# Kernel optimization log

Hardware: AMD Instinct MI355X
Metric: run time of the kernel (lower is better)

The kernel has to match this reference:

```python
import jax, jax.numpy as jnp
import numpy as np

N_NODES = 50000
N_EDGES = 800000
IN_FT = 256
OUT_FT = 128


def setup_inputs() -> dict:
    key = jax.random.key(0)
    k_seq, k_src, k_dst, k_val, k_w = jax.random.split(key, 5)
    seq = jax.random.normal(k_seq, (N_NODES, IN_FT), dtype=jnp.float32)
    edge_src = jax.random.randint(k_src, (N_EDGES,), 0, N_NODES, dtype=jnp.int64)
    edge_dst = jax.random.randint(k_dst, (N_EDGES,), 0, N_NODES, dtype=jnp.int64)
    edge_val = jax.random.uniform(k_val, (N_EDGES,), dtype=jnp.float32)
    # xavier_uniform for Linear(in_ft, out_ft): limit = sqrt(6/(in+out))
    limit = float(np.sqrt(6.0 / (IN_FT + OUT_FT)))
    W = jax.random.uniform(k_w, (OUT_FT, IN_FT), minval=-limit, maxval=limit, dtype=jnp.float32)
    bias = jnp.zeros((OUT_FT,), dtype=jnp.float32)
    prelu_a = jnp.full((1,), 0.25, dtype=jnp.float32)  # nn.PReLU default slope
    return {"seq": seq, "edge_src": edge_src, "edge_dst": edge_dst,
            "edge_val": edge_val, "W": W, "bias": bias, "prelu_a": prelu_a}


def reference(seq, edge_src, edge_dst, edge_val, W, bias, prelu_a):
    # seq_fts = fc(seq): [N, out_ft]
    seq_fts = jnp.einsum('ni,oi->no', seq, W)
    # sparse spmm: out[dst] += val * seq_fts[src]
    msgs = seq_fts[edge_src] * edge_val[:, None]          # [E, out_ft]
    out = jax.ops.segment_sum(msgs, edge_dst, num_segments=seq.shape[0])
    out = out + bias                                       # bias add
    # PReLU with learnable slope a
    return jnp.where(out >= 0, out, prelu_a * out)
```

## Files before the change

### kernel.cpp

```cpp
#include <hip/hip_runtime.h>
#include <hip/hip_bf16.h>

#define N_NODES 50000
#define N_EDGES 800000
#define IN_FT 256
#define OUT_FT 128

typedef __bf16 bf16;
typedef __attribute__((ext_vector_type(8))) __bf16 bf16x8;
typedef __attribute__((ext_vector_type(4))) float floatx4;

static __device__ inline unsigned short f2bf_bits(float f) {
    unsigned u = __float_as_uint(f);
    return (unsigned short)((u + 0x7FFFu + ((u >> 16) & 1u)) >> 16);
}

#define SLOT_LG 6
#define SLOTS (1 << SLOT_LG)
#define BKN 128
#define NBUCK 392
#define NPAD (NBUCK * BKN)
#define EPB 2048
#define NBLK_A ((N_EDGES + EPB - 1) / EPB)
#define CELL 32
#define SXCAP 2560
#define GM 128
#define GEMM_BLKS ((N_NODES + GM - 1) / GM)
#define WP 264
#define SMEM_BYTES (128 * WP * 2)

__global__ __launch_bounds__(512) void k_ga(const float* __restrict__ seq,
                                            const float* __restrict__ W,
                                            unsigned short* __restrict__ seq_fts,
                                            const int* __restrict__ src,
                                            const int* __restrict__ dst,
                                            const float* __restrict__ val,
                                            int* __restrict__ cnt,
                                            uint2* __restrict__ part) {
    const int t = threadIdx.x;
    __shared__ __align__(16) char smem[SMEM_BYTES];
    if (blockIdx.x < GEMM_BLKS) {
        bf16* Wlds = (bf16*)smem;
        {
            const int row = t >> 2, c0 = (t & 3) * 64;
            const float* wsrc = W + row * IN_FT + c0;
            unsigned short* dstp = (unsigned short*)(Wlds + row * WP + c0);
#pragma unroll
            for (int c = 0; c < 16; ++c) {
                float4 v = *(const float4*)(wsrc + c * 4);
                ushort4 o;
                o.x = f2bf_bits(v.x); o.y = f2bf_bits(v.y);
                o.z = f2bf_bits(v.z); o.w = f2bf_bits(v.w);
                *(ushort4*)(dstp + c * 4) = o;
            }
        }
        const int lane = t & 63;
        const int wave = t >> 6;
        const int quad = lane >> 4;
        const int l16  = lane & 15;

        int arow = blockIdx.x * GM + wave * 16 + l16;
        if (arow >= N_NODES) arow = 0;
        const float* ap = seq + (size_t)arow * IN_FT + quad * 8;
        bf16x8 afr[8];
#pragma unroll
        for (int s = 0; s < 8; ++s) {
            float4 v0 = *(const float4*)(ap + s * 32);
            float4 v1 = *(const float4*)(ap + s * 32 + 4);
            bf16x8 a;
            a[0] = (bf16)v0.x; a[1] = (bf16)v0.y; a[2] = (bf16)v0.z; a[3] = (bf16)v0.w;
            a[4] = (bf16)v1.x; a[5] = (bf16)v1.y; a[6] = (bf16)v1.z; a[7] = (bf16)v1.w;
            afr[s] = a;
        }
        __syncthreads();

        const int mbase = blockIdx.x * GM + wave * 16;
#pragma unroll
        for (int tt = 0; tt < 8; ++tt) {
            floatx4 acc = {0.f, 0.f, 0.f, 0.f};
            const bf16* bp = Wlds + (tt * 16 + l16) * WP + quad * 8;
#pragma unroll
            for (int s = 0; s < 8; ++s) {
                bf16x8 bfr = *(const bf16x8*)(bp + s * 32);
                acc = __builtin_amdgcn_mfma_f32_16x16x32_bf16(afr[s], bfr, acc, 0, 0, 0);
            }
#pragma unroll
            for (int r = 0; r < 4; ++r) {
                int m = mbase + quad * 4 + r;
                if (m < N_NODES)
                    seq_fts[(size_t)m * OUT_FT + tt * 16 + l16] = f2bf_bits(acc[r]);
            }
        }
    } else {
        int*   h     = (int*)smem;
        int*   lbase = h + NBUCK;
        int*   sc    = lbase + NBUCK;
        uint2* srt   = (uint2*)(sc + 512);

        const int B2 = blockIdx.x - GEMM_BLKS;
        const int e0 = B2 * EPB;
        if (t < NBUCK) h[t] = 0;
        __syncthreads();

        int      myd[4];
        int      myofs[4];
        unsigned myx[4];
#pragma unroll
        for (int k = 0; k < 4; ++k) {
            int e = e0 + k * 512 + t;
            int d = (e < N_EDGES) ? dst[e] : -1;
            myd[k] = d;
            if (d >= 0) {
                myx[k] = (unsigned)(unsigned short)src[e]
                       | ((unsigned)f2bf_bits(val[e]) << 16);
                myofs[k] = atomicAdd(&h[d >> 7], 1);
            }
        }
        __syncthreads();
        int v = (t < NBUCK) ? min(h[t], CELL) : 0;
        sc[t] = v;
        __syncthreads();
        for (int s = 1; s < 512; s <<= 1) {
            int a = (t >= s) ? sc[t - s] : 0;
            __syncthreads();
            sc[t] += a;
            __syncthreads();
        }
        if (t < NBUCK) { lbase[t] = sc[t] - v; cnt[t * NBLK_A + B2] = v; }
        __syncthreads();
        const int total = sc[NBUCK - 1];
#pragma unroll
        for (int k = 0; k < 4; ++k) {
            int d = myd[k];
            if (d >= 0 && myofs[k] < CELL)
                srt[lbase[d >> 7] + myofs[k]] = make_uint2(myx[k], (unsigned)d);
        }
        __syncthreads();
        for (int i = t; i < total; i += 512) {
            uint2 r = srt[i];
            int bb = (int)(r.y >> 7);
            part[(size_t)(bb * NBLK_A + B2) * CELL + (unsigned)(i - lbase[bb])] = r;
        }
    }
}

__global__ __launch_bounds__(512) void k_B(const int* __restrict__ cnt,
                                           const uint2* __restrict__ part,
                                           unsigned* __restrict__ csr_ev,
                                           int* __restrict__ deg) {
    const int b = blockIdx.x, t = threadIdx.x;
    __shared__ int sc[512];
    __shared__ int ncnt[BKN], nbase[BKN], ncur[BKN];
    __shared__ int tot_sh;
    __shared__ unsigned fx[SXCAP];
    __shared__ unsigned char fdn[SXCAP];
    __shared__ unsigned sx[SXCAP];
    __shared__ unsigned char sdn[SXCAP];

    if (t < BKN) ncnt[t] = 0;
    const int len = (t < NBLK_A) ? cnt[b * NBLK_A + t] : 0;
    sc[t] = len;
    __syncthreads();
    for (int s = 1; s < 512; s <<= 1) {
        int a = (t >= s) ? sc[t - s] : 0;
        __syncthreads();
        sc[t] += a;
        __syncthreads();
    }
    const int cellbase = sc[t] - len;
    if (t == NBLK_A - 1) tot_sh = sc[NBLK_A - 1];
    __syncthreads();
    const int totc = (tot_sh < SXCAP) ? tot_sh : SXCAP;

    if (t < NBLK_A) {
        const uint2* cp = part + (size_t)(b * NBLK_A + t) * CELL;
        for (int k = 0; k < len; ++k) {
            int idx = cellbase + k;
            if (idx < SXCAP) {
                uint2 r = cp[k];
                int dn = (int)(r.y & (BKN - 1));
                fx[idx] = r.x;
                fdn[idx] = (unsigned char)dn;
                atomicAdd(&ncnt[dn], 1);
            }
        }
    }
    __syncthreads();
    int v2 = (t < BKN) ? ncnt[t] : 0;
    if (t < BKN) sc[t] = v2;
    __syncthreads();
    for (int s = 1; s < BKN; s <<= 1) {
        int a = (t < BKN && t >= s) ? sc[t - s] : 0;
        __syncthreads();
        if (t < BKN) sc[t] += a;
        __syncthreads();
    }
    if (t < BKN) {
        nbase[t] = sc[t] - v2;
        ncur[t]  = sc[t] - v2;
        deg[b * BKN + t] = (v2 < SLOTS) ? v2 : SLOTS;
    }
    __syncthreads();
    for (int i = t; i < totc; i += 512) {
        unsigned x = fx[i];
        int dn = fdn[i];
        int j = atomicAdd(&ncur[dn], 1);
        sx[j] = x; sdn[j] = (unsigned char)dn;
    }
    __syncthreads();
    for (int j = t; j < totc; j += 512) {
        int dn = sdn[j];
        int lpos = j - nbase[dn];
        if (lpos < SLOTS)
            csr_ev[((unsigned)(b * BKN + dn) << SLOT_LG) + (unsigned)lpos] = sx[j];
    }
}

#define GW 4
__global__ __launch_bounds__(64 * GW) void k_gather(const unsigned* __restrict__ fts,
                                                    const int* __restrict__ deg,
                                                    const unsigned* __restrict__ csr_ev,
                                                    const float* __restrict__ bias,
                                                    const float* __restrict__ prelu_a,
                                                    float* __restrict__ out) {
    const int wave = threadIdx.x >> 6;
    const int lane = threadIdx.x & 63;
    const int n = blockIdx.x * GW + wave;
    if (n >= N_NODES) return;
    const int d = deg[n];
    const int s0 = n << SLOT_LG;
    const int s1 = s0 + d;
    float acc0 = 0.f, acc1 = 0.f;
    int j = s0;
    for (; j + 7 < s1; j += 8) {
        uint4 ca = *(const uint4*)&csr_ev[j];
        uint4 cb = *(const uint4*)&csr_ev[j + 4];
        unsigned q0 = fts[(ca.x & 0xFFFFu) * 64u + lane];
        unsigned q1 = fts[(ca.y & 0xFFFFu) * 64u + lane];
        unsigned q2 = fts[(ca.z & 0xFFFFu) * 64u + lane];
        unsigned q3 = fts[(ca.w & 0xFFFFu) * 64u + lane];
        unsigned q4 = fts[(cb.x & 0xFFFFu) * 64u + lane];
        unsigned q5 = fts[(cb.y & 0xFFFFu) * 64u + lane];
        unsigned q6 = fts[(cb.z & 0xFFFFu) * 64u + lane];
        unsigned q7 = fts[(cb.w & 0xFFFFu) * 64u + lane];
        acc0 += __uint_as_float(ca.x & 0xFFFF0000u) * __uint_as_float(q0 << 16);
        acc1 += __uint_as_float(ca.x & 0xFFFF0000u) * __uint_as_float(q0 & 0xFFFF0000u);
        acc0 += __uint_as_float(ca.y & 0xFFFF0000u) * __uint_as_float(q1 << 16);
        acc1 += __uint_as_float(ca.y & 0xFFFF0000u) * __uint_as_float(q1 & 0xFFFF0000u);
        acc0 += __uint_as_float(ca.z & 0xFFFF0000u) * __uint_as_float(q2 << 16);
        acc1 += __uint_as_float(ca.z & 0xFFFF0000u) * __uint_as_float(q2 & 0xFFFF0000u);
        acc0 += __uint_as_float(ca.w & 0xFFFF0000u) * __uint_as_float(q3 << 16);
        acc1 += __uint_as_float(ca.w & 0xFFFF0000u) * __uint_as_float(q3 & 0xFFFF0000u);
        acc0 += __uint_as_float(cb.x & 0xFFFF0000u) * __uint_as_float(q4 << 16);
        acc1 += __uint_as_float(cb.x & 0xFFFF0000u) * __uint_as_float(q4 & 0xFFFF0000u);
        acc0 += __uint_as_float(cb.y & 0xFFFF0000u) * __uint_as_float(q5 << 16);
        acc1 += __uint_as_float(cb.y & 0xFFFF0000u) * __uint_as_float(q5 & 0xFFFF0000u);
        acc0 += __uint_as_float(cb.z & 0xFFFF0000u) * __uint_as_float(q6 << 16);
        acc1 += __uint_as_float(cb.z & 0xFFFF0000u) * __uint_as_float(q6 & 0xFFFF0000u);
        acc0 += __uint_as_float(cb.w & 0xFFFF0000u) * __uint_as_float(q7 << 16);
        acc1 += __uint_as_float(cb.w & 0xFFFF0000u) * __uint_as_float(q7 & 0xFFFF0000u);
    }
    for (; j + 3 < s1; j += 4) {
        uint4 ca = *(const uint4*)&csr_ev[j];
        unsigned q0 = fts[(ca.x & 0xFFFFu) * 64u + lane];
        unsigned q1 = fts[(ca.y & 0xFFFFu) * 64u + lane];
        unsigned q2 = fts[(ca.z & 0xFFFFu) * 64u + lane];
        unsigned q3 = fts[(ca.w & 0xFFFFu) * 64u + lane];
        acc0 += __uint_as_float(ca.x & 0xFFFF0000u) * __uint_as_float(q0 << 16);
        acc1 += __uint_as_float(ca.x & 0xFFFF0000u) * __uint_as_float(q0 & 0xFFFF0000u);
        acc0 += __uint_as_float(ca.y & 0xFFFF0000u) * __uint_as_float(q1 << 16);
        acc1 += __uint_as_float(ca.y & 0xFFFF0000u) * __uint_as_float(q1 & 0xFFFF0000u);
        acc0 += __uint_as_float(ca.z & 0xFFFF0000u) * __uint_as_float(q2 << 16);
        acc1 += __uint_as_float(ca.z & 0xFFFF0000u) * __uint_as_float(q2 & 0xFFFF0000u);
        acc0 += __uint_as_float(ca.w & 0xFFFF0000u) * __uint_as_float(q3 << 16);
        acc1 += __uint_as_float(ca.w & 0xFFFF0000u) * __uint_as_float(q3 & 0xFFFF0000u);
    }
    for (; j < s1; ++j) {
        unsigned w0 = csr_ev[j];
        unsigned p0 = fts[(w0 & 0xFFFFu) * 64u + lane];
        float v0 = __uint_as_float(w0 & 0xFFFF0000u);
        acc0 += v0 * __uint_as_float(p0 << 16);
        acc1 += v0 * __uint_as_float(p0 & 0xFFFF0000u);
    }
    float2 bb = *(const float2*)&bias[lane * 2];
    float a = prelu_a[0];
    float x0 = acc0 + bb.x;
    float x1 = acc1 + bb.y;
    x0 = (x0 >= 0.f) ? x0 : a * x0;
    x1 = (x1 >= 0.f) ? x1 : a * x1;
    *(float2*)&out[(size_t)n * OUT_FT + lane * 2] = make_float2(x0, x1);
}

extern "C" void kernel_launch(void* const* d_in, const int* in_sizes, int n_in,
                              void* d_out, int out_size, void* d_ws, size_t ws_size,
                              hipStream_t stream) {
    const float* seq      = (const float*)d_in[0];
    const int*   edge_src = (const int*)d_in[1];
    const int*   edge_dst = (const int*)d_in[2];
    const float* edge_val = (const float*)d_in[3];
    const float* W        = (const float*)d_in[4];
    const float* bias     = (const float*)d_in[5];
    const float* prelu_a  = (const float*)d_in[6];
    float* out = (float*)d_out;

    char* ws = (char*)d_ws;
    size_t off = 0;
    auto alloc = [&](size_t bytes) {
        void* p = ws + off;
        off = (off + bytes + 255) & ~(size_t)255;
        return p;
    };
    unsigned short* seq_fts = (unsigned short*)alloc((size_t)N_NODES * OUT_FT * sizeof(unsigned short));
    int*      cnt    = (int*)alloc((size_t)NBUCK * NBLK_A * sizeof(int));
    uint2*    part   = (uint2*)alloc((size_t)NBUCK * NBLK_A * CELL * sizeof(uint2));
    unsigned* csr_ev = (unsigned*)alloc((size_t)NPAD * SLOTS * sizeof(unsigned));
    int*      deg    = (int*)alloc((size_t)NPAD * sizeof(int));
    (void)ws_size; (void)in_sizes; (void)n_in; (void)out_size;

    k_ga<<<GEMM_BLKS + NBLK_A, 512, 0, stream>>>(seq, W, seq_fts,
                                                 edge_src, edge_dst, edge_val,
                                                 cnt, part);
    k_B<<<NBUCK, 512, 0, stream>>>(cnt, part, csr_ev, deg);
    k_gather<<<(N_NODES + GW - 1) / GW, 64 * GW, 0, stream>>>((const unsigned*)seq_fts,
                                                              deg, csr_ev,
                                                              bias, prelu_a, out);
}
```

Before: 169.5 us.

## Fuse bucket sort and gather into one kernel reading edges from LDS

Merges the per-bucket local sort kernel and the per-node gather kernel into one 1024-thread kernel. After the sort, 16 waves per block walk the 128 nodes of the bucket, reading edge records straight from shared memory. This drops the padded global CSR buffer, the degree array, their global write and read round trip, and one kernel launch. It also removes the 64-edge per-node cap. In exchange the gather runs with only 392 large blocks instead of many small ones, which lowers parallelism and load balancing for a latency-bound random gather.

```diff
diff --git a/kernel.cpp b/kernel.cpp
--- a/kernel.cpp
+++ b/kernel.cpp
@@ -15,8 +15,6 @@
     return (unsigned short)((u + 0x7FFFu + ((u >> 16) & 1u)) >> 16);
 }
 
-#define SLOT_LG 6
-#define SLOTS (1 << SLOT_LG)
 #define BKN 128
 #define NBUCK 392
 #define NPAD (NBUCK * BKN)
@@ -144,12 +142,15 @@
     }
 }
 
-__global__ __launch_bounds__(512) void k_B(const int* __restrict__ cnt,
-                                           const uint2* __restrict__ part,
-                                           unsigned* __restrict__ csr_ev,
-                                           int* __restrict__ deg) {
+#define NW 16
+__global__ __launch_bounds__(1024) void k_BG(const int* __restrict__ cnt,
+                                             const uint2* __restrict__ part,
+                                             const unsigned* __restrict__ fts,
+                                             const float* __restrict__ bias,
+                                             const float* __restrict__ prelu_a,
+                                             float* __restrict__ out) {
     const int b = blockIdx.x, t = threadIdx.x;
-    __shared__ int sc[512];
+    __shared__ int sc[1024];
     __shared__ int ncnt[BKN], nbase[BKN], ncur[BKN];
     __shared__ int tot_sh;
     __shared__ unsigned fx[SXCAP];
@@ -198,97 +199,86 @@
     if (t < BKN) {
         nbase[t] = sc[t] - v2;
         ncur[t]  = sc[t] - v2;
-        deg[b * BKN + t] = (v2 < SLOTS) ? v2 : SLOTS;
-    }
-    __syncthreads();
-    for (int i = t; i < totc; i += 512) {
+    }
+    __syncthreads();
+    for (int i = t; i < totc; i += 1024) {
         unsigned x = fx[i];
         int dn = fdn[i];
         int j = atomicAdd(&ncur[dn], 1);
         sx[j] = x; sdn[j] = (unsigned char)dn;
     }
     __syncthreads();
-    for (int j = t; j < totc; j += 512) {
-        int dn = sdn[j];
-        int lpos = j - nbase[dn];
-        if (lpos < SLOTS)
-            csr_ev[((unsigned)(b * BKN + dn) << SLOT_LG) + (unsigned)lpos] = sx[j];
-    }
-}
-
-#define GW 4
-__global__ __launch_bounds__(64 * GW) void k_gather(const unsigned* __restrict__ fts,
-                                                    const int* __restrict__ deg,
-                                                    const unsigned* __restrict__ csr_ev,
-                                                    const float* __restrict__ bias,
-                                                    const float* __restrict__ prelu_a,
-                                                    float* __restrict__ out) {
-    const int wave = threadIdx.x >> 6;
-    const int lane = threadIdx.x & 63;
-    const int n = blockIdx.x * GW + wave;
-    if (n >= N_NODES) return;
-    const int d = deg[n];
-    const int s0 = n << SLOT_LG;
-    const int s1 = s0 + d;
-    float acc0 = 0.f, acc1 = 0.f;
-    int j = s0;
-    for (; j + 7 < s1; j += 8) {
-        uint4 ca = *(const uint4*)&csr_ev[j];
-        uint4 cb = *(const uint4*)&csr_ev[j + 4];
-        unsigned q0 = fts[(ca.x & 0xFFFFu) * 64u + lane];
-        unsigned q1 = fts[(ca.y & 0xFFFFu) * 64u + lane];
-        unsigned q2 = fts[(ca.z & 0xFFFFu) * 64u + lane];
-        unsigned q3 = fts[(ca.w & 0xFFFFu) * 64u + lane];
-        unsigned q4 = fts[(cb.x & 0xFFFFu) * 64u + lane];
-        unsigned q5 = fts[(cb.y & 0xFFFFu) * 64u + lane];
-        unsigned q6 = fts[(cb.z & 0xFFFFu) * 64u + lane];
-        unsigned q7 = fts[(cb.w & 0xFFFFu) * 64u + lane];
-        acc0 += __uint_as_float(ca.x & 0xFFFF0000u) * __uint_as_float(q0 << 16);
-        acc1 += __uint_as_float(ca.x & 0xFFFF0000u) * __uint_as_float(q0 & 0xFFFF0000u);
-        acc0 += __uint_as_float(ca.y & 0xFFFF0000u) * __uint_as_float(q1 << 16);
-        acc1 += __uint_as_float(ca.y & 0xFFFF0000u) * __uint_as_float(q1 & 0xFFFF0000u);
-        acc0 += __uint_as_float(ca.z & 0xFFFF0000u) * __uint_as_float(q2 << 16);
-        acc1 += __uint_as_float(ca.z & 0xFFFF0000u) * __uint_as_float(q2 & 0xFFFF0000u);
-        acc0 += __uint_as_float(ca.w & 0xFFFF0000u) * __uint_as_float(q3 << 16);
-        acc1 += __uint_as_float(ca.w & 0xFFFF0000u) * __uint_as_float(q3 & 0xFFFF0000u);
-        acc0 += __uint_as_float(cb.x & 0xFFFF0000u) * __uint_as_float(q4 << 16);
-        acc1 += __uint_as_float(cb.x & 0xFFFF0000u) * __uint_as_float(q4 & 0xFFFF0000u);
-        acc0 += __uint_as_float(cb.y & 0xFFFF0000u) * __uint_as_float(q5 << 16);
-        acc1 += __uint_as_float(cb.y & 0xFFFF0000u) * __uint_as_float(q5 & 0xFFFF0000u);
-        acc0 += __uint_as_float(cb.z & 0xFFFF0000u) * __uint_as_float(q6 << 16);
-        acc1 += __uint_as_float(cb.z & 0xFFFF0000u) * __uint_as_float(q6 & 0xFFFF0000u);
-        acc0 += __uint_as_float(cb.w & 0xFFFF0000u) * __uint_as_float(q7 << 16);
-        acc1 += __uint_as_float(cb.w & 0xFFFF0000u) * __uint_as_float(q7 & 0xFFFF0000u);
-    }
-    for (; j + 3 < s1; j += 4) {
-        uint4 ca = *(const uint4*)&csr_ev[j];
-        unsigned q0 = fts[(ca.x & 0xFFFFu) * 64u + lane];
-        unsigned q1 = fts[(ca.y & 0xFFFFu) * 64u + lane];
-        unsigned q2 = fts[(ca.z & 0xFFFFu) * 64u + lane];
-        unsigned q3 = fts[(ca.w & 0xFFFFu) * 64u + lane];
-        acc0 += __uint_as_float(ca.x & 0xFFFF0000u) * __uint_as_float(q0 << 16);
-        acc1 += __uint_as_float(ca.x & 0xFFFF0000u) * __uint_as_float(q0 & 0xFFFF0000u);
-        acc0 += __uint_as_float(ca.y & 0xFFFF0000u) * __uint_as_float(q1 << 16);
-        acc1 += __uint_as_float(ca.y & 0xFFFF0000u) * __uint_as_float(q1 & 0xFFFF0000u);
-        acc0 += __uint_as_float(ca.z & 0xFFFF0000u) * __uint_as_float(q2 << 16);
-        acc1 += __uint_as_float(ca.z & 0xFFFF0000u) * __uint_as_float(q2 & 0xFFFF0000u);
-        acc0 += __uint_as_float(ca.w & 0xFFFF0000u) * __uint_as_float(q3 << 16);
-        acc1 += __uint_as_float(ca.w & 0xFFFF0000u) * __uint_as_float(q3 & 0xFFFF0000u);
-    }
-    for (; j < s1; ++j) {
-        unsigned w0 = csr_ev[j];
-        unsigned p0 = fts[(w0 & 0xFFFFu) * 64u + lane];
-        float v0 = __uint_as_float(w0 & 0xFFFF0000u);
-        acc0 += v0 * __uint_as_float(p0 << 16);
-        acc1 += v0 * __uint_as_float(p0 & 0xFFFF0000u);
-    }
-    float2 bb = *(const float2*)&bias[lane * 2];
-    float a = prelu_a[0];
-    float x0 = acc0 + bb.x;
-    float x1 = acc1 + bb.y;
-    x0 = (x0 >= 0.f) ? x0 : a * x0;
-    x1 = (x1 >= 0.f) ? x1 : a * x1;
-    *(float2*)&out[(size_t)n * OUT_FT + lane * 2] = make_float2(x0, x1);
+
+    const int wave = t >> 6;
+    const int lane = t & 63;
+    const float2 bb2 = *(const float2*)&bias[lane * 2];
+    const float a = prelu_a[0];
+    for (int ln = wave; ln < BKN; ln += NW) {
+        const int n = b * BKN + ln;
+        if (n >= N_NODES) continue;
+        const int s0 = nbase[ln];
+        const int s1 = s0 + ncnt[ln];
+        float acc0 = 0.f, acc1 = 0.f;
+        int j = s0;
+        for (; j + 7 < s1; j += 8) {
+            unsigned x0 = sx[j],     x1 = sx[j + 1];
+            unsigned x2 = sx[j + 2], x3 = sx[j + 3];
+            unsigned x4 = sx[j + 4], x5 = sx[j + 5];
+            unsigned x6 = sx[j + 6], x7 = sx[j + 7];
+            unsigned q0 = fts[(x0 & 0xFFFFu) * 64u + lane];
+            unsigned q1 = fts[(x1 & 0xFFFFu) * 64u + lane];
+            unsigned q2 = fts[(x2 & 0xFFFFu) * 64u + lane];
+            unsigned q3 = fts[(x3 & 0xFFFFu) * 64u + lane];
+            unsigned q4 = fts[(x4 & 0xFFFFu) * 64u + lane];
+            unsigned q5 = fts[(x5 & 0xFFFFu) * 64u + lane];
+            unsigned q6 = fts[(x6 & 0xFFFFu) * 64u + lane];
+            unsigned q7 = fts[(x7 & 0xFFFFu) * 64u + lane];
+            acc0 += __uint_as_float(x0 & 0xFFFF0000u) * __uint_as_float(q0 << 16);
+            acc1 += __uint_as_float(x0 & 0xFFFF0000u) * __uint_as_float(q0 & 0xFFFF0000u);
+            acc0 += __uint_as_float(x1 & 0xFFFF0000u) * __uint_as_float(q1 << 16);
+            acc1 += __uint_as_float(x1 & 0xFFFF0000u) * __uint_as_float(q1 & 0xFFFF0000u);
+            acc0 += __uint_as_float(x2 & 0xFFFF0000u) * __uint_as_float(q2 << 16);
+            acc1 += __uint_as_float(x2 & 0xFFFF0000u) * __uint_as_float(q2 & 0xFFFF0000u);
+            acc0 += __uint_as_float(x3 & 0xFFFF0000u) * __uint_as_float(q3 << 16);
+            acc1 += __uint_as_float(x3 & 0xFFFF0000u) * __uint_as_float(q3 & 0xFFFF0000u);
+            acc0 += __uint_as_float(x4 & 0xFFFF0000u) * __uint_as_float(q4 << 16);
+            acc1 += __uint_as_float(x4 & 0xFFFF0000u) * __uint_as_float(q4 & 0xFFFF0000u);
+            acc0 += __uint_as_float(x5 & 0xFFFF0000u) * __uint_as_float(q5 << 16);
+            acc1 += __uint_as_float(x5 & 0xFFFF0000u) * __uint_as_float(q5 & 0xFFFF0000u);
+            acc0 += __uint_as_float(x6 & 0xFFFF0000u) * __uint_as_float(q6 << 16);
+            acc1 += __uint_as_float(x6 & 0xFFFF0000u) * __uint_as_float(q6 & 0xFFFF0000u);
+            acc0 += __uint_as_float(x7 & 0xFFFF0000u) * __uint_as_float(q7 << 16);
+            acc1 += __uint_as_float(x7 & 0xFFFF0000u) * __uint_as_float(q7 & 0xFFFF0000u);
+        }
+        for (; j + 3 < s1; j += 4) {
+            unsigned x0 = sx[j],     x1 = sx[j + 1];
+            unsigned x2 = sx[j + 2], x3 = sx[j + 3];
+            unsigned q0 = fts[(x0 & 0xFFFFu) * 64u + lane];
+            unsigned q1 = fts[(x1 & 0xFFFFu) * 64u + lane];
+            unsigned q2 = fts[(x2 & 0xFFFFu) * 64u + lane];
+            unsigned q3 = fts[(x3 & 0xFFFFu) * 64u + lane];
+            acc0 += __uint_as_float(x0 & 0xFFFF0000u) * __uint_as_float(q0 << 16);
+            acc1 += __uint_as_float(x0 & 0xFFFF0000u) * __uint_as_float(q0 & 0xFFFF0000u);
+            acc0 += __uint_as_float(x1 & 0xFFFF0000u) * __uint_as_float(q1 << 16);
+            acc1 += __uint_as_float(x1 & 0xFFFF0000u) * __uint_as_float(q1 & 0xFFFF0000u);
+            acc0 += __uint_as_float(x2 & 0xFFFF0000u) * __uint_as_float(q2 << 16);
+            acc1 += __uint_as_float(x2 & 0xFFFF0000u) * __uint_as_float(q2 & 0xFFFF0000u);
+            acc0 += __uint_as_float(x3 & 0xFFFF0000u) * __uint_as_float(q3 << 16);
+            acc1 += __uint_as_float(x3 & 0xFFFF0000u) * __uint_as_float(q3 & 0xFFFF0000u);
+        }
+        for (; j < s1; ++j) {
+            unsigned x0 = sx[j];
+            unsigned q0 = fts[(x0 & 0xFFFFu) * 64u + lane];
+            float v0 = __uint_as_float(x0 & 0xFFFF0000u);
+            acc0 += v0 * __uint_as_float(q0 << 16);
+            acc1 += v0 * __uint_as_float(q0 & 0xFFFF0000u);
+        }
+        float x0f = acc0 + bb2.x;
+        float x1f = acc1 + bb2.y;
+        x0f = (x0f >= 0.f) ? x0f : a * x0f;
+        x1f = (x1f >= 0.f) ? x1f : a * x1f;
+        *(float2*)&out[(size_t)n * OUT_FT + lane * 2] = make_float2(x0f, x1f);
+    }
 }
 
 extern "C" void kernel_launch(void* const* d_in, const int* in_sizes, int n_in,
@@ -311,17 +301,13 @@
         return p;
     };
     unsigned short* seq_fts = (unsigned short*)alloc((size_t)N_NODES * OUT_FT * sizeof(unsigned short));
-    int*      cnt    = (int*)alloc((size_t)NBUCK * NBLK_A * sizeof(int));
-    uint2*    part   = (uint2*)alloc((size_t)NBUCK * NBLK_A * CELL * sizeof(uint2));
-    unsigned* csr_ev = (unsigned*)alloc((size_t)NPAD * SLOTS * sizeof(unsigned));
-    int*      deg    = (int*)alloc((size_t)NPAD * sizeof(int));
+    int*   cnt  = (int*)alloc((size_t)NBUCK * NBLK_A * sizeof(int));
+    uint2* part = (uint2*)alloc((size_t)NBUCK * NBLK_A * CELL * sizeof(uint2));
     (void)ws_size; (void)in_sizes; (void)n_in; (void)out_size;
 
     k_ga<<<GEMM_BLKS + NBLK_A, 512, 0, stream>>>(seq, W, seq_fts,
                                                  edge_src, edge_dst, edge_val,
                                                  cnt, part);
-    k_B<<<NBUCK, 512, 0, stream>>>(cnt, part, csr_ev, deg);
-    k_gather<<<(N_NODES + GW - 1) / GW, 64 * GW, 0, stream>>>((const unsigned*)seq_fts,
-                                                              deg, csr_ev,
-                                                              bias, prelu_a, out);
+    k_BG<<<NBUCK, 1024, 0, stream>>>(cnt, part, (const unsigned*)seq_fts,
+                                     bias, prelu_a, out);
 }
```

New measurement: 158.7 us. -6.4%, faster.
